# Optimization experiments

Hardware: AMD Instinct MI355X
Metric: run time of the kernel (lower is better)

## Reference

```python
import jax, jax.numpy as jnp
import numpy as np

D = 8        # num_decoders
N = 65536    # num_entries
LAT = 64     # latent_dim
HID = 128    # hidden_dim_dec
FEAT = 16    # feature_dim


def setup_inputs() -> dict:
    key = jax.random.key(0)
    ks = jax.random.split(key, 6)
    return {
        "weight": jax.random.normal(ks[0], (N, LAT), jnp.float32) * 2.0,
        "alpha_param": jax.random.normal(ks[1], (D, N), jnp.float32),  # alpha_std=1.0
        "div": jnp.ones((LAT,), jnp.float32),
        "scale0": jax.random.normal(ks[2], (D, LAT, HID), jnp.float32),  # ldec_std=1.0 normal init
        "shift0": jnp.zeros((D, 1, HID), jnp.float32),
        "scale1": jax.random.normal(ks[3], (D, HID, HID), jnp.float32),
        "shift1": jnp.zeros((D, 1, HID), jnp.float32),
        "scale2": jax.random.normal(ks[4], (D, HID, FEAT), jnp.float32),
        "shift2": jnp.zeros((D, 1, FEAT), jnp.float32),
    }


def _st_round(x):
    # StraightThrough: round in forward, identity gradient
    return x + jax.lax.stop_gradient(jnp.round(x) - x)


def _layer(x, alpha, scale, shift):
    # x: [N, I], alpha: [D, N], scale: [D, I, O], shift: [D, 1, O]
    out = jnp.einsum('ni,dio->dno', x, scale)           # per-decoder GEMMs [D,N,O]
    mix = jnp.einsum('dno,dn->no', out, alpha)          # alpha-weighted combine
    # second alpha-weighted sum over (mix + per-decoder shift), as in the torch code
    return jnp.einsum('dno,dn->no', mix[None, :, :] + shift, alpha)


def reference(weight, alpha_param, div, scale0, shift0, scale1, shift1, scale2, shift2):
    temperature = 1.0
    a = jax.nn.softmax(alpha_param / temperature, axis=0)       # [D, N]
    idx = jnp.argmax(a, axis=0)                                 # [N]
    onehot = jax.nn.one_hot(idx, a.shape[0], dtype=a.dtype).T   # [D, N]
    alpha = a + jax.lax.stop_gradient(onehot - a)               # straight-through one-hot

    x = _st_round(weight) / div                                 # [N, LAT]
    x = jax.nn.relu(_layer(x, alpha, scale0, shift0))           # [N, HID]
    x = jax.nn.relu(_layer(x, alpha, scale1, shift1))           # [N, HID]
    out = _layer(x, alpha, scale2, shift2)                      # [N, FEAT], final_activation='none'
    return out
```

## Files before the change

kernel.cpp:

```cpp
#include <hip/hip_runtime.h>

#define NN 65536
#define DD 8
#define LATD 64
#define HIDD 128
#define FEATD 16
#define BPD 64
#define STRH 136
#define STRS0 72

typedef __attribute__((ext_vector_type(8))) short short8;
typedef __attribute__((ext_vector_type(4))) float f32x4;
typedef __attribute__((ext_vector_type(8))) unsigned short ushort8;

static __device__ __forceinline__ unsigned short f2bf(float f) {
  union { float f; unsigned u; } v; v.f = f;
  unsigned r = v.u + 0x7FFFu + ((v.u >> 16) & 1u);
  return (unsigned short)(r >> 16);
}

__global__ __launch_bounds__(256) void k_bucket(const float* __restrict__ ap,
                                                int* __restrict__ cursor,
                                                unsigned short* __restrict__ perm) {
  __shared__ int bc[DD];
  __shared__ int bbase[DD];
  int t = threadIdx.x;
  if (t < DD) bc[t] = 0;
  __syncthreads();
  int n = blockIdx.x * 256 + t;
  float best = ap[n];
  int bd = 0;
#pragma unroll
  for (int d = 1; d < DD; ++d) {
    float v = ap[d * NN + n];
    if (v > best) { best = v; bd = d; }
  }
  int lr = atomicAdd(&bc[bd], 1);
  __syncthreads();
  if (t < DD) bbase[t] = atomicAdd(&cursor[t], bc[t]);
  __syncthreads();
  perm[bd * NN + bbase[bd] + lr] = (unsigned short)n;
}

__global__ __launch_bounds__(256) void k_convert(const float* __restrict__ s0,
                                                 const float* __restrict__ s1,
                                                 const float* __restrict__ s2,
                                                 unsigned short* __restrict__ g0,
                                                 unsigned short* __restrict__ g1,
                                                 unsigned short* __restrict__ g2) {
  int o = blockIdx.x * 256 + threadIdx.x;
  if (o < DD * HIDD * LATD) {
    int d = o >> 13, rem = o & 8191, n = rem >> 6, k = rem & 63;
    g0[o] = f2bf(s0[d * 8192 + k * 128 + n]);
  }
  if (o < DD * HIDD * HIDD) {
    int d = o >> 14, rem = o & 16383, n = rem >> 7, k = rem & 127;
    g1[o] = f2bf(s1[d * 16384 + k * 128 + n]);
  }
  if (o < DD * FEATD * HIDD) {
    int d = o >> 11, rem = o & 2047, n = rem >> 7, k = rem & 127;
    g2[o] = f2bf(s2[d * 2048 + k * 16 + n]);
  }
}

__global__ __launch_bounds__(256, 2) void k_mlp(
    const float* __restrict__ weight, const float* __restrict__ divv,
    const float* __restrict__ shift0, const float* __restrict__ shift1,
    const float* __restrict__ shift2,
    const int* __restrict__ cursor, const unsigned short* __restrict__ perm,
    const unsigned short* __restrict__ g0, const unsigned short* __restrict__ g1,
    const unsigned short* __restrict__ g2,
    float* __restrict__ out) {
  __shared__ unsigned short sH[64 * STRH];
  __shared__ unsigned short s0T[128 * STRS0];
  __shared__ unsigned short s1T[128 * STRH];
  __shared__ unsigned short s2T[16 * STRH];

  int d = blockIdx.x / BPD;
  int bslot = blockIdx.x % BPD;
  int cnt = cursor[d];
  int t = threadIdx.x;
  int w = t >> 6, l = t & 63;
  int lrow = l & 15, kgrp = l >> 4;

  {
    const ushort8* src0 = (const ushort8*)(g0 + d * (HIDD * LATD));
#pragma unroll
    for (int c = 0; c < 4; ++c) {
      int lin = c * 256 + t, r = lin >> 3, wi = lin & 7;
      *(ushort8*)&s0T[r * STRS0 + wi * 8] = src0[lin];
    }
    const ushort8* src1 = (const ushort8*)(g1 + d * (HIDD * HIDD));
#pragma unroll
    for (int c = 0; c < 8; ++c) {
      int lin = c * 256 + t, r = lin >> 4, wi = lin & 15;
      *(ushort8*)&s1T[r * STRH + wi * 8] = src1[lin];
    }
    const ushort8* src2 = (const ushort8*)(g2 + d * (FEATD * HIDD));
    {
      int r = t >> 4, wi = t & 15;
      *(ushort8*)&s2T[r * STRH + wi * 8] = src2[t];
    }
  }
  __syncthreads();

  float sh2v = shift2[d * FEATD + lrow];

  for (int tile = bslot; tile * 64 < cnt; tile += BPD) {
    int base = tile * 64;
    int nvalid = min(64, cnt - base);

    int arow = base + w * 16 + lrow;
    short8 xa[2];
#pragma unroll
    for (int s = 0; s < 2; ++s) {
      short8 v;
      if (arow < cnt) {
        int e = (int)perm[d * NN + arow];
        const float* wr = weight + e * LATD + s * 32 + kgrp * 8;
        const float* dv = divv + s * 32 + kgrp * 8;
        float4 f0 = *(const float4*)wr;
        float4 f1 = *(const float4*)(wr + 4);
        float4 q0 = *(const float4*)dv;
        float4 q1 = *(const float4*)(dv + 4);
        v[0] = (short)f2bf(rintf(f0.x) / q0.x);
        v[1] = (short)f2bf(rintf(f0.y) / q0.y);
        v[2] = (short)f2bf(rintf(f0.z) / q0.z);
        v[3] = (short)f2bf(rintf(f0.w) / q0.w);
        v[4] = (short)f2bf(rintf(f1.x) / q1.x);
        v[5] = (short)f2bf(rintf(f1.y) / q1.y);
        v[6] = (short)f2bf(rintf(f1.z) / q1.z);
        v[7] = (short)f2bf(rintf(f1.w) / q1.w);
      } else {
#pragma unroll
        for (int j = 0; j < 8; ++j) v[j] = 0;
      }
      xa[s] = v;
    }

#pragma unroll
    for (int tt = 0; tt < 8; ++tt) {
      float sh = shift0[d * HIDD + tt * 16 + lrow];
      f32x4 acc = {sh, sh, sh, sh};
      short8 b0 = *(short8*)&s0T[(tt * 16 + lrow) * STRS0 + kgrp * 8];
      short8 b1 = *(short8*)&s0T[(tt * 16 + lrow) * STRS0 + 32 + kgrp * 8];
      acc = __builtin_amdgcn_mfma_f32_16x16x32_bf16(xa[0], b0, acc, 0, 0, 0);
      acc = __builtin_amdgcn_mfma_f32_16x16x32_bf16(xa[1], b1, acc, 0, 0, 0);
#pragma unroll
      for (int r = 0; r < 4; ++r)
        sH[(w * 16 + kgrp * 4 + r) * STRH + tt * 16 + lrow] = f2bf(fmaxf(acc[r], 0.f));
    }

    short8 ha[4];
#pragma unroll
    for (int s = 0; s < 4; ++s)
      ha[s] = *(short8*)&sH[(w * 16 + lrow) * STRH + s * 32 + kgrp * 8];
#pragma unroll
    for (int tt = 0; tt < 8; ++tt) {
      float sh = shift1[d * HIDD + tt * 16 + lrow];
      f32x4 acc = {sh, sh, sh, sh};
#pragma unroll
      for (int s = 0; s < 4; ++s) {
        short8 b = *(short8*)&s1T[(tt * 16 + lrow) * STRH + s * 32 + kgrp * 8];
        acc = __builtin_amdgcn_mfma_f32_16x16x32_bf16(ha[s], b, acc, 0, 0, 0);
      }
#pragma unroll
      for (int r = 0; r < 4; ++r)
        sH[(w * 16 + kgrp * 4 + r) * STRH + tt * 16 + lrow] = f2bf(fmaxf(acc[r], 0.f));
    }

    short8 ga[4];
#pragma unroll
    for (int s = 0; s < 4; ++s)
      ga[s] = *(short8*)&sH[(w * 16 + lrow) * STRH + s * 32 + kgrp * 8];
    f32x4 acc = {sh2v, sh2v, sh2v, sh2v};
#pragma unroll
    for (int s = 0; s < 4; ++s) {
      short8 b = *(short8*)&s2T[lrow * STRH + s * 32 + kgrp * 8];
      acc = __builtin_amdgcn_mfma_f32_16x16x32_bf16(ga[s], b, acc, 0, 0, 0);
    }
#pragma unroll
    for (int r = 0; r < 4; ++r) {
      int p = base + w * 16 + kgrp * 4 + r;
      if (p < cnt) {
        int e = (int)perm[d * NN + p];
        out[e * FEATD + lrow] = acc[r];
      }
    }
    (void)nvalid;
  }
}

extern "C" void kernel_launch(void* const* d_in, const int* in_sizes, int n_in,
                              void* d_out, int out_size, void* d_ws, size_t ws_size,
                              hipStream_t stream) {
  const float* weight      = (const float*)d_in[0];
  const float* alpha_param = (const float*)d_in[1];
  const float* divv        = (const float*)d_in[2];
  const float* scale0      = (const float*)d_in[3];
  const float* shift0      = (const float*)d_in[4];
  const float* scale1      = (const float*)d_in[5];
  const float* shift1      = (const float*)d_in[6];
  const float* scale2      = (const float*)d_in[7];
  const float* shift2      = (const float*)d_in[8];
  float* out = (float*)d_out;

  int* cursor = (int*)d_ws;
  unsigned short* perm = (unsigned short*)((int*)d_ws + 8);
  unsigned short* g0 = perm + DD * NN;
  unsigned short* g1 = g0 + DD * HIDD * LATD;
  unsigned short* g2 = g1 + DD * HIDD * HIDD;

  hipMemsetAsync(cursor, 0, DD * sizeof(int), stream);
  k_bucket<<<NN / 256, 256, 0, stream>>>(alpha_param, cursor, perm);
  k_convert<<<(DD * HIDD * HIDD) / 256, 256, 0, stream>>>(scale0, scale1, scale2, g0, g1, g2);
  k_mlp<<<DD * BPD, 256, 0, stream>>>(weight, divv, shift0, shift1, shift2,
                                      cursor, perm, g0, g1, g2, out);
}
```

Baseline: 36.51 us.

## Keep decoder weights in registers and drop separate bf16 convert kernel

Removes the k_convert launch. Each wave now loads and converts its slice of the per-decoder scale matrices straight from fp32 global memory into registers, instead of staging them in LDS. The work split changes so each wave owns 32 output columns across all 64 rows of a tile, with the x tile and hidden activations shared through LDS behind block barriers. Blocks per decoder rise from 64 to 96 with a target of 3 blocks per CU, trading more registers and three barriers per tile for less LDS use and one fewer launch. The strided scalar fp32 weight loads in the prologue are uncoalesced and are repeated by every block.

```diff
diff --git a/kernel.cpp b/kernel.cpp
--- a/kernel.cpp
+++ b/kernel.cpp
@@ -5,13 +5,12 @@
 #define LATD 64
 #define HIDD 128
 #define FEATD 16
-#define BPD 64
-#define STRH 136
-#define STRS0 72
+#define BPD 96
+#define SXS 72
+#define SHS 136
 
 typedef __attribute__((ext_vector_type(8))) short short8;
 typedef __attribute__((ext_vector_type(4))) float f32x4;
-typedef __attribute__((ext_vector_type(8))) unsigned short ushort8;
 
 static __device__ __forceinline__ unsigned short f2bf(float f) {
   union { float f; unsigned u; } v; v.f = f;
@@ -42,152 +41,158 @@
   perm[bd * NN + bbase[bd] + lr] = (unsigned short)n;
 }
 
-__global__ __launch_bounds__(256) void k_convert(const float* __restrict__ s0,
-                                                 const float* __restrict__ s1,
-                                                 const float* __restrict__ s2,
-                                                 unsigned short* __restrict__ g0,
-                                                 unsigned short* __restrict__ g1,
-                                                 unsigned short* __restrict__ g2) {
-  int o = blockIdx.x * 256 + threadIdx.x;
-  if (o < DD * HIDD * LATD) {
-    int d = o >> 13, rem = o & 8191, n = rem >> 6, k = rem & 63;
-    g0[o] = f2bf(s0[d * 8192 + k * 128 + n]);
-  }
-  if (o < DD * HIDD * HIDD) {
-    int d = o >> 14, rem = o & 16383, n = rem >> 7, k = rem & 127;
-    g1[o] = f2bf(s1[d * 16384 + k * 128 + n]);
-  }
-  if (o < DD * FEATD * HIDD) {
-    int d = o >> 11, rem = o & 2047, n = rem >> 7, k = rem & 127;
-    g2[o] = f2bf(s2[d * 2048 + k * 16 + n]);
-  }
-}
-
-__global__ __launch_bounds__(256, 2) void k_mlp(
+__global__ __launch_bounds__(256, 3) void k_mlp(
     const float* __restrict__ weight, const float* __restrict__ divv,
-    const float* __restrict__ shift0, const float* __restrict__ shift1,
-    const float* __restrict__ shift2,
+    const float* __restrict__ s0, const float* __restrict__ sh0,
+    const float* __restrict__ s1, const float* __restrict__ sh1,
+    const float* __restrict__ s2, const float* __restrict__ sh2,
     const int* __restrict__ cursor, const unsigned short* __restrict__ perm,
-    const unsigned short* __restrict__ g0, const unsigned short* __restrict__ g1,
-    const unsigned short* __restrict__ g2,
     float* __restrict__ out) {
-  __shared__ unsigned short sH[64 * STRH];
-  __shared__ unsigned short s0T[128 * STRS0];
-  __shared__ unsigned short s1T[128 * STRH];
-  __shared__ unsigned short s2T[16 * STRH];
-
-  int d = blockIdx.x / BPD;
-  int bslot = blockIdx.x % BPD;
+  __shared__ unsigned short sX[64 * SXS];
+  __shared__ unsigned short sH1[64 * SHS];
+  __shared__ unsigned short sH2[64 * SHS];
+  __shared__ unsigned short sP[64];
+
+  int d = blockIdx.x / BPD, bslot = blockIdx.x % BPD;
   int cnt = cursor[d];
   int t = threadIdx.x;
   int w = t >> 6, l = t & 63;
   int lrow = l & 15, kgrp = l >> 4;
 
-  {
-    const ushort8* src0 = (const ushort8*)(g0 + d * (HIDD * LATD));
-#pragma unroll
-    for (int c = 0; c < 4; ++c) {
-      int lin = c * 256 + t, r = lin >> 3, wi = lin & 7;
-      *(ushort8*)&s0T[r * STRS0 + wi * 8] = src0[lin];
-    }
-    const ushort8* src1 = (const ushort8*)(g1 + d * (HIDD * HIDD));
-#pragma unroll
-    for (int c = 0; c < 8; ++c) {
-      int lin = c * 256 + t, r = lin >> 4, wi = lin & 15;
-      *(ushort8*)&s1T[r * STRH + wi * 8] = src1[lin];
-    }
-    const ushort8* src2 = (const ushort8*)(g2 + d * (FEATD * HIDD));
-    {
-      int r = t >> 4, wi = t & 15;
-      *(ushort8*)&s2T[r * STRH + wi * 8] = src2[t];
-    }
-  }
-  __syncthreads();
-
-  float sh2v = shift2[d * FEATD + lrow];
+  short8 b0[2][2];
+  short8 b1[2][4];
+  short8 b2[4];
+  float sh0v[2], sh1v[2];
+  const float* S0 = s0 + d * LATD * HIDD;
+  const float* S1 = s1 + d * HIDD * HIDD;
+  const float* S2 = s2 + d * HIDD * FEATD;
+#pragma unroll
+  for (int cb = 0; cb < 2; ++cb) {
+    int n = (2 * w + cb) * 16 + lrow;
+#pragma unroll
+    for (int ks = 0; ks < 2; ++ks) {
+      short8 v;
+#pragma unroll
+      for (int j = 0; j < 8; ++j)
+        v[j] = (short)f2bf(S0[(ks * 32 + kgrp * 8 + j) * HIDD + n]);
+      b0[cb][ks] = v;
+    }
+#pragma unroll
+    for (int ks = 0; ks < 4; ++ks) {
+      short8 v;
+#pragma unroll
+      for (int j = 0; j < 8; ++j)
+        v[j] = (short)f2bf(S1[(ks * 32 + kgrp * 8 + j) * HIDD + n]);
+      b1[cb][ks] = v;
+    }
+    sh0v[cb] = sh0[d * HIDD + n];
+    sh1v[cb] = sh1[d * HIDD + n];
+  }
+#pragma unroll
+  for (int ks = 0; ks < 4; ++ks) {
+    short8 v;
+#pragma unroll
+    for (int j = 0; j < 8; ++j)
+      v[j] = (short)f2bf(S2[(ks * 32 + kgrp * 8 + j) * FEATD + lrow]);
+    b2[ks] = v;
+  }
+  float sh2v = sh2[d * FEATD + lrow];
 
   for (int tile = bslot; tile * 64 < cnt; tile += BPD) {
     int base = tile * 64;
-    int nvalid = min(64, cnt - base);
-
-    int arow = base + w * 16 + lrow;
-    short8 xa[2];
-#pragma unroll
-    for (int s = 0; s < 2; ++s) {
-      short8 v;
-      if (arow < cnt) {
-        int e = (int)perm[d * NN + arow];
-        const float* wr = weight + e * LATD + s * 32 + kgrp * 8;
-        const float* dv = divv + s * 32 + kgrp * 8;
-        float4 f0 = *(const float4*)wr;
-        float4 f1 = *(const float4*)(wr + 4);
-        float4 q0 = *(const float4*)dv;
-        float4 q1 = *(const float4*)(dv + 4);
-        v[0] = (short)f2bf(rintf(f0.x) / q0.x);
-        v[1] = (short)f2bf(rintf(f0.y) / q0.y);
-        v[2] = (short)f2bf(rintf(f0.z) / q0.z);
-        v[3] = (short)f2bf(rintf(f0.w) / q0.w);
-        v[4] = (short)f2bf(rintf(f1.x) / q1.x);
-        v[5] = (short)f2bf(rintf(f1.y) / q1.y);
-        v[6] = (short)f2bf(rintf(f1.z) / q1.z);
-        v[7] = (short)f2bf(rintf(f1.w) / q1.w);
-      } else {
-#pragma unroll
-        for (int j = 0; j < 8; ++j) v[j] = 0;
-      }
-      xa[s] = v;
-    }
-
-#pragma unroll
-    for (int tt = 0; tt < 8; ++tt) {
-      float sh = shift0[d * HIDD + tt * 16 + lrow];
-      f32x4 acc = {sh, sh, sh, sh};
-      short8 b0 = *(short8*)&s0T[(tt * 16 + lrow) * STRS0 + kgrp * 8];
-      short8 b1 = *(short8*)&s0T[(tt * 16 + lrow) * STRS0 + 32 + kgrp * 8];
-      acc = __builtin_amdgcn_mfma_f32_16x16x32_bf16(xa[0], b0, acc, 0, 0, 0);
-      acc = __builtin_amdgcn_mfma_f32_16x16x32_bf16(xa[1], b1, acc, 0, 0, 0);
-#pragma unroll
-      for (int r = 0; r < 4; ++r)
-        sH[(w * 16 + kgrp * 4 + r) * STRH + tt * 16 + lrow] = f2bf(fmaxf(acc[r], 0.f));
-    }
-
-    short8 ha[4];
-#pragma unroll
-    for (int s = 0; s < 4; ++s)
-      ha[s] = *(short8*)&sH[(w * 16 + lrow) * STRH + s * 32 + kgrp * 8];
-#pragma unroll
-    for (int tt = 0; tt < 8; ++tt) {
-      float sh = shift1[d * HIDD + tt * 16 + lrow];
-      f32x4 acc = {sh, sh, sh, sh};
-#pragma unroll
-      for (int s = 0; s < 4; ++s) {
-        short8 b = *(short8*)&s1T[(tt * 16 + lrow) * STRH + s * 32 + kgrp * 8];
-        acc = __builtin_amdgcn_mfma_f32_16x16x32_bf16(ha[s], b, acc, 0, 0, 0);
-      }
-#pragma unroll
-      for (int r = 0; r < 4; ++r)
-        sH[(w * 16 + kgrp * 4 + r) * STRH + tt * 16 + lrow] = f2bf(fmaxf(acc[r], 0.f));
-    }
-
-    short8 ga[4];
-#pragma unroll
-    for (int s = 0; s < 4; ++s)
-      ga[s] = *(short8*)&sH[(w * 16 + lrow) * STRH + s * 32 + kgrp * 8];
-    f32x4 acc = {sh2v, sh2v, sh2v, sh2v};
-#pragma unroll
-    for (int s = 0; s < 4; ++s) {
-      short8 b = *(short8*)&s2T[lrow * STRH + s * 32 + kgrp * 8];
-      acc = __builtin_amdgcn_mfma_f32_16x16x32_bf16(ga[s], b, acc, 0, 0, 0);
-    }
-#pragma unroll
-    for (int r = 0; r < 4; ++r) {
-      int p = base + w * 16 + kgrp * 4 + r;
-      if (p < cnt) {
-        int e = (int)perm[d * NN + p];
-        out[e * FEATD + lrow] = acc[r];
-      }
-    }
-    (void)nvalid;
+
+    {
+      int r = t >> 2, c = t & 3;
+      int gp = base + r;
+      unsigned short pe = 0;
+      short8 lo = {0, 0, 0, 0, 0, 0, 0, 0}, hi = {0, 0, 0, 0, 0, 0, 0, 0};
+      if (gp < cnt) {
+        pe = perm[d * NN + gp];
+        const float* wr = weight + (int)pe * LATD + c * 16;
+        const float* dv = divv + c * 16;
+#pragma unroll
+        for (int q = 0; q < 2; ++q) {
+          float4 f = *(const float4*)(wr + q * 4);
+          float4 g = *(const float4*)(dv + q * 4);
+          lo[q * 4 + 0] = (short)f2bf(rintf(f.x) / g.x);
+          lo[q * 4 + 1] = (short)f2bf(rintf(f.y) / g.y);
+          lo[q * 4 + 2] = (short)f2bf(rintf(f.z) / g.z);
+          lo[q * 4 + 3] = (short)f2bf(rintf(f.w) / g.w);
+        }
+#pragma unroll
+        for (int q = 0; q < 2; ++q) {
+          float4 f = *(const float4*)(wr + 8 + q * 4);
+          float4 g = *(const float4*)(dv + 8 + q * 4);
+          hi[q * 4 + 0] = (short)f2bf(rintf(f.x) / g.x);
+          hi[q * 4 + 1] = (short)f2bf(rintf(f.y) / g.y);
+          hi[q * 4 + 2] = (short)f2bf(rintf(f.z) / g.z);
+          hi[q * 4 + 3] = (short)f2bf(rintf(f.w) / g.w);
+        }
+      }
+      if (c == 0) sP[r] = pe;
+      *(short8*)&sX[r * SXS + c * 16] = lo;
+      *(short8*)&sX[r * SXS + c * 16 + 8] = hi;
+    }
+    __syncthreads();
+
+    int prow[4];
+#pragma unroll
+    for (int rr = 0; rr < 4; ++rr) prow[rr] = (int)sP[w * 16 + kgrp * 4 + rr];
+
+#pragma unroll
+    for (int rg = 0; rg < 4; ++rg) {
+      short8 a0 = *(short8*)&sX[(rg * 16 + lrow) * SXS + kgrp * 8];
+      short8 a1 = *(short8*)&sX[(rg * 16 + lrow) * SXS + 32 + kgrp * 8];
+#pragma unroll
+      for (int cb = 0; cb < 2; ++cb) {
+        f32x4 acc = {sh0v[cb], sh0v[cb], sh0v[cb], sh0v[cb]};
+        acc = __builtin_amdgcn_mfma_f32_16x16x32_bf16(a0, b0[cb][0], acc, 0, 0, 0);
+        acc = __builtin_amdgcn_mfma_f32_16x16x32_bf16(a1, b0[cb][1], acc, 0, 0, 0);
+#pragma unroll
+        for (int rr = 0; rr < 4; ++rr)
+          sH1[(rg * 16 + kgrp * 4 + rr) * SHS + (2 * w + cb) * 16 + lrow] =
+              f2bf(fmaxf(acc[rr], 0.f));
+      }
+    }
+    __syncthreads();
+
+#pragma unroll
+    for (int rg = 0; rg < 4; ++rg) {
+      short8 h0 = *(short8*)&sH1[(rg * 16 + lrow) * SHS + kgrp * 8];
+      short8 h1 = *(short8*)&sH1[(rg * 16 + lrow) * SHS + 32 + kgrp * 8];
+      short8 h2 = *(short8*)&sH1[(rg * 16 + lrow) * SHS + 64 + kgrp * 8];
+      short8 h3 = *(short8*)&sH1[(rg * 16 + lrow) * SHS + 96 + kgrp * 8];
+#pragma unroll
+      for (int cb = 0; cb < 2; ++cb) {
+        f32x4 acc = {sh1v[cb], sh1v[cb], sh1v[cb], sh1v[cb]};
+        acc = __builtin_amdgcn_mfma_f32_16x16x32_bf16(h0, b1[cb][0], acc, 0, 0, 0);
+        acc = __builtin_amdgcn_mfma_f32_16x16x32_bf16(h1, b1[cb][1], acc, 0, 0, 0);
+        acc = __builtin_amdgcn_mfma_f32_16x16x32_bf16(h2, b1[cb][2], acc, 0, 0, 0);
+        acc = __builtin_amdgcn_mfma_f32_16x16x32_bf16(h3, b1[cb][3], acc, 0, 0, 0);
+#pragma unroll
+        for (int rr = 0; rr < 4; ++rr)
+          sH2[(rg * 16 + kgrp * 4 + rr) * SHS + (2 * w + cb) * 16 + lrow] =
+              f2bf(fmaxf(acc[rr], 0.f));
+      }
+    }
+    __syncthreads();
+
+    {
+      short8 g0 = *(short8*)&sH2[(w * 16 + lrow) * SHS + kgrp * 8];
+      short8 g1 = *(short8*)&sH2[(w * 16 + lrow) * SHS + 32 + kgrp * 8];
+      short8 g2 = *(short8*)&sH2[(w * 16 + lrow) * SHS + 64 + kgrp * 8];
+      short8 g3 = *(short8*)&sH2[(w * 16 + lrow) * SHS + 96 + kgrp * 8];
+      f32x4 acc = {sh2v, sh2v, sh2v, sh2v};
+      acc = __builtin_amdgcn_mfma_f32_16x16x32_bf16(g0, b2[0], acc, 0, 0, 0);
+      acc = __builtin_amdgcn_mfma_f32_16x16x32_bf16(g1, b2[1], acc, 0, 0, 0);
+      acc = __builtin_amdgcn_mfma_f32_16x16x32_bf16(g2, b2[2], acc, 0, 0, 0);
+      acc = __builtin_amdgcn_mfma_f32_16x16x32_bf16(g3, b2[3], acc, 0, 0, 0);
+#pragma unroll
+      for (int rr = 0; rr < 4; ++rr) {
+        int row = w * 16 + kgrp * 4 + rr;
+        if (base + row < cnt) out[prow[rr] * FEATD + lrow] = acc[rr];
+      }
+    }
   }
 }
 
@@ -207,13 +212,11 @@
 
   int* cursor = (int*)d_ws;
   unsigned short* perm = (unsigned short*)((int*)d_ws + 8);
-  unsigned short* g0 = perm + DD * NN;
-  unsigned short* g1 = g0 + DD * HIDD * LATD;
-  unsigned short* g2 = g1 + DD * HIDD * HIDD;
 
   hipMemsetAsync(cursor, 0, DD * sizeof(int), stream);
   k_bucket<<<NN / 256, 256, 0, stream>>>(alpha_param, cursor, perm);
-  k_convert<<<(DD * HIDD * HIDD) / 256, 256, 0, stream>>>(scale0, scale1, scale2, g0, g1, g2);
-  k_mlp<<<DD * BPD, 256, 0, stream>>>(weight, divv, shift0, shift1, shift2,
-                                      cursor, perm, g0, g1, g2, out);
-}
+  k_mlp<<<DD * BPD, 256, 0, stream>>>(weight, divv,
+                                      scale0, shift0, scale1, shift1,
+                                      scale2, shift2,
+                                      cursor, perm, out);
+}
```

Result: faster. 30.34 us (-16.9%).
